# Kernel optimization log

Measured on AMD Instinct MI355X. Metric: run time of the kernel, lower is better.

## Reference

```python
import jax, jax.numpy as jnp
import numpy as np

N_EMBED = 1024
N_HEADS = 16
HEAD = N_EMBED // N_HEADS
EPS = 1e-5


def setup_inputs() -> dict:
    key = jax.random.key(0)
    ks = jax.random.split(key, 16)
    C = N_EMBED
    s = lambda fan_in: 1.0 / np.sqrt(fan_in)
    return {
        "x": jax.random.normal(ks[0], (4, 2048, C), jnp.float32),
        "ln1_g": jnp.ones((C,), jnp.float32),
        "ln1_b": jnp.zeros((C,), jnp.float32),
        "w_attn": jax.random.normal(ks[1], (C, 3 * C), jnp.float32) * s(C),
        "b_attn": jnp.zeros((3 * C,), jnp.float32),
        "w_proj": jax.random.normal(ks[2], (C, C), jnp.float32) * s(C),
        "b_proj": jnp.zeros((C,), jnp.float32),
        "ln2_g": jnp.ones((C,), jnp.float32),
        "ln2_b": jnp.zeros((C,), jnp.float32),
        "w_fc": jax.random.normal(ks[3], (C, 4 * C), jnp.float32) * s(C),
        "b_fc": jnp.zeros((4 * C,), jnp.float32),
        "w_fc2": jax.random.normal(ks[4], (4 * C, C), jnp.float32) * s(4 * C),
        "b_fc2": jnp.zeros((C,), jnp.float32),
    }


def _layernorm(x, g, b):
    mu = jnp.mean(x, axis=-1, keepdims=True)
    var = jnp.mean(jnp.square(x - mu), axis=-1, keepdims=True)
    return (x - mu) * jax.lax.rsqrt(var + EPS) * g + b


def _attention(x, w_attn, b_attn, w_proj, b_proj):
    B, T, C = x.shape
    qkv = x @ w_attn + b_attn  # [B,T,3C]
    q, k, v = jnp.split(qkv, 3, axis=-1)
    q = q.reshape(B, T, N_HEADS, HEAD).transpose(0, 2, 1, 3)  # [B,H,T,D]
    k = k.reshape(B, T, N_HEADS, HEAD).transpose(0, 2, 1, 3)
    v = v.reshape(B, T, N_HEADS, HEAD).transpose(0, 2, 1, 3)
    scale = 1.0 / np.sqrt(HEAD)
    affin = jnp.einsum("bhqd,bhkd->bhqk", q, k) * scale  # [B,H,T,T]
    causal = jnp.tril(jnp.ones((T, T), bool))
    affin = jnp.where(causal, affin, -jnp.inf)
    affin = jax.nn.softmax(affin, axis=-1)
    y = jnp.einsum("bhqk,bhkd->bhqd", affin, v)  # [B,H,T,D]
    y = y.transpose(0, 2, 1, 3).reshape(B, T, C)
    return y @ w_proj + b_proj


def reference(x, ln1_g, ln1_b, w_attn, b_attn, w_proj, b_proj,
              ln2_g, ln2_b, w_fc, b_fc, w_fc2, b_fc2):
    x = x + _attention(_layernorm(x, ln1_g, ln1_b), w_attn, b_attn, w_proj, b_proj)
    h = _layernorm(x, ln2_g, ln2_b)
    h = jax.nn.gelu(h @ w_fc + b_fc, approximate=True)  # tanh GELU
    x = x + (h @ w_fc2 + b_fc2)
    return x
```

## Files before the change

### kernel.cpp

```cpp
#include <hip/hip_runtime.h>
#include <math.h>


#define M_ROWS 8192
#define T_SEQ 2048
#define N_EMB 1024
#define N_HEADS 16
#define HEAD_D 64

typedef _Float16 f16;
typedef __attribute__((ext_vector_type(8))) _Float16 f16x8;
typedef __attribute__((ext_vector_type(4))) _Float16 f16x4;
typedef __attribute__((ext_vector_type(4))) float f32x4;

__device__ __forceinline__ void async16(void* lds, const void* g) {
    __builtin_amdgcn_global_load_lds(
        (const __attribute__((address_space(1))) unsigned int*)g,
        (__attribute__((address_space(3))) unsigned int*)lds, 16, 0, 0);
}

__device__ __forceinline__ float gelu_tanh(float v) {
    float u = 0.7978845608028654f * (v + 0.044715f * v * v * v);
    float e = __expf(2.0f * u);
    float t = 1.0f - 2.0f / (e + 1.0f);
    return 0.5f * v * (1.0f + t);
}

__launch_bounds__(256)
__global__ void wconv_kernel(const float* __restrict__ W, f16* __restrict__ WT,
                             int K, int N) {
    __shared__ float t[32][33];
    int tx = threadIdx.x & 31, ty = threadIdx.x >> 5;
    int n0 = blockIdx.x * 32, k0 = blockIdx.y * 32;
    #pragma unroll
    for (int r = 0; r < 4; r++)
        t[ty * 4 + r][tx] = W[(size_t)(k0 + ty * 4 + r) * N + n0 + tx];
    __syncthreads();
    #pragma unroll
    for (int r = 0; r < 4; r++)
        WT[(size_t)(n0 + ty * 4 + r) * K + k0 + tx] = (f16)t[tx][ty * 4 + r];
}

__launch_bounds__(256)
__global__ void ln_kernel(const float* __restrict__ x, const float* __restrict__ g,
                          const float* __restrict__ b, f16* __restrict__ y) {
    int row = blockIdx.x;
    int tid = threadIdx.x;
    const float* xr = x + (size_t)row * N_EMB;
    float4 v = *(const float4*)(xr + tid * 4);
    float s  = v.x + v.y + v.z + v.w;
    float sq = v.x * v.x + v.y * v.y + v.z * v.z + v.w * v.w;
    #pragma unroll
    for (int off = 32; off > 0; off >>= 1) {
        s  += __shfl_down(s, off);
        sq += __shfl_down(sq, off);
    }
    __shared__ float ws_[4], wq_[4];
    __shared__ float mean_s, rstd_s;
    int lane = tid & 63, wid = tid >> 6;
    if (lane == 0) { ws_[wid] = s; wq_[wid] = sq; }
    __syncthreads();
    if (tid == 0) {
        float st = ws_[0] + ws_[1] + ws_[2] + ws_[3];
        float qt = wq_[0] + wq_[1] + wq_[2] + wq_[3];
        float mu = st * (1.0f / N_EMB);
        float var = qt * (1.0f / N_EMB) - mu * mu;
        mean_s = mu;
        rstd_s = rsqrtf(var + 1e-5f);
    }
    __syncthreads();
    float mu = mean_s, r = rstd_s;
    float4 gv = *(const float4*)(g + tid * 4);
    float4 bv = *(const float4*)(b + tid * 4);
    f16x4 o;
    o.x = (f16)((v.x - mu) * r * gv.x + bv.x);
    o.y = (f16)((v.y - mu) * r * gv.y + bv.y);
    o.z = (f16)((v.z - mu) * r * gv.z + bv.z);
    o.w = (f16)((v.w - mu) * r * gv.w + bv.w);
    *(f16x4*)(y + (size_t)row * N_EMB + tid * 4) = o;
}

template <int EPI>
__launch_bounds__(256)
__global__ void gemm_f16(const f16* __restrict__ A, const f16* __restrict__ Bt,
                         const float* __restrict__ bias, const float* __restrict__ res,
                         float* __restrict__ Cf, f16* __restrict__ Ch,
                         f16* __restrict__ vT, int K, int N) {
    __shared__ f16 As[3][128 * 32];
    __shared__ f16 Bs[3][128 * 32];
    int tid = threadIdx.x;
    int lane = tid & 63, wave = tid >> 6;
    int wr = wave >> 1, wc = wave & 1;
    int quad = lane >> 4, l16 = lane & 15;

    int nx = gridDim.x;
    int nwg = nx * gridDim.y;
    int orig = blockIdx.y * nx + blockIdx.x;
    int cpx = nwg >> 3;
    int swz = (orig & 7) * cpx + (orig >> 3);
    int m0 = (swz / nx) * 128, n0 = (swz % nx) * 128;

    int r0 = tid >> 2;
    int s0 = (tid & 3) * 8;
    const f16* paA0 = A  + (size_t)(m0 + r0) * K + s0;
    const f16* paA1 = A  + (size_t)(m0 + r0 + 64) * K + s0;
    const f16* paB0 = Bt + (size_t)(n0 + r0) * K + s0;
    const f16* paB1 = Bt + (size_t)(n0 + r0 + 64) * K + s0;
    char* sA0 = (char*)As + (size_t)tid * 16;
    char* sA1 = (char*)As + (size_t)(256 + tid) * 16;
    char* sB0 = (char*)Bs + (size_t)tid * 16;
    char* sB1 = (char*)Bs + (size_t)(256 + tid) * 16;

    int nt = K >> 5;

    {
        async16(sA0, paA0); async16(sA1, paA1);
        async16(sB0, paB0); async16(sB1, paB1);
        async16(sA0 + 8192, paA0 + 32); async16(sA1 + 8192, paA1 + 32);
        async16(sB0 + 8192, paB0 + 32); async16(sB1 + 8192, paB1 + 32);
    }

    f32x4 acc[4][4] = {};
    int bc = 0;
    for (int t = 0; t < nt; t++) {
        if (t + 2 < nt) {
            int b2 = bc ? bc - 1 : 2;
            size_t bo = (size_t)b2 * 8192;
            int koff = (t + 2) * 32;
            async16(sA0 + bo, paA0 + koff); async16(sA1 + bo, paA1 + koff);
            async16(sB0 + bo, paB0 + koff); async16(sB1 + bo, paB1 + koff);
            asm volatile("s_waitcnt vmcnt(8)" ::: "memory");
        } else if (t + 2 == nt) {
            asm volatile("s_waitcnt vmcnt(4)" ::: "memory");
        } else {
            asm volatile("s_waitcnt vmcnt(0)" ::: "memory");
        }
        __builtin_amdgcn_s_barrier();

        const f16* as = As[bc];
        const f16* bs = Bs[bc];
        f16x8 af[4], bf[4];
        #pragma unroll
        for (int i = 0; i < 4; i++)
            af[i] = *(const f16x8*)&as[(wr * 64 + i * 16 + l16) * 32 + quad * 8];
        #pragma unroll
        for (int j = 0; j < 4; j++)
            bf[j] = *(const f16x8*)&bs[(wc * 64 + j * 16 + l16) * 32 + quad * 8];
        __builtin_amdgcn_s_setprio(1);
        #pragma unroll
        for (int i = 0; i < 4; i++)
            #pragma unroll
            for (int j = 0; j < 4; j++)
                acc[i][j] = __builtin_amdgcn_mfma_f32_16x16x32_f16(
                    af[i], bf[j], acc[i][j], 0, 0, 0);
        __builtin_amdgcn_s_setprio(0);
        __builtin_amdgcn_s_barrier();
        bc = (bc == 2) ? 0 : bc + 1;
    }

    #pragma unroll
    for (int i = 0; i < 4; i++) {
        int row0 = m0 + wr * 64 + i * 16 + quad * 4;
        #pragma unroll
        for (int j = 0; j < 4; j++) {
            int col = n0 + wc * 64 + j * 16 + l16;
            float bb = bias[col];
            if (EPI == 3) {
                if (n0 < 2048) {
                    #pragma unroll
                    for (int r = 0; r < 4; r++)
                        Ch[(size_t)(row0 + r) * 2048 + col] = (f16)(acc[i][j][r] + bb);
                } else {
                    int hh = (col - 2048) >> 6, dd = col & 63;
                    int bb_ = row0 >> 11, t0 = row0 & 2047;
                    f16x4 pk;
                    pk.x = (f16)(acc[i][j][0] + bb);
                    pk.y = (f16)(acc[i][j][1] + bb);
                    pk.z = (f16)(acc[i][j][2] + bb);
                    pk.w = (f16)(acc[i][j][3] + bb);
                    *(f16x4*)(vT + ((size_t)(bb_ * 16 + hh) * 64 + dd) * 2048 + t0) = pk;
                }
            } else {
                #pragma unroll
                for (int r = 0; r < 4; r++) {
                    size_t idx = (size_t)(row0 + r) * N + col;
                    float v = acc[i][j][r] + bb;
                    if (EPI == 1) v += res[idx];
                    if (EPI == 2) Ch[idx] = (f16)gelu_tanh(v);
                    else          Cf[idx] = v;
                }
            }
        }
    }
}

__launch_bounds__(256, 2)
__global__ void flash_kernel(const f16* __restrict__ qk, const f16* __restrict__ vT,
                             f16* __restrict__ y) {
    __shared__ __align__(16) char smem[67584];
    f16* Ks = (f16*)smem;
    f16* Vs = (f16*)(smem + 16384);
    int tid = threadIdx.x;
    int lane = tid & 63, w = tid >> 6;
    int quad = lane >> 4, l16 = lane & 15;
    f16* Ps = (f16*)(smem + 32768 + w * 8704);

    int bh = blockIdx.y;
    int b = bh >> 4, h = bh & 15;

    for (int half = 0; half < 2; half++) {
        int qt = half ? (int)blockIdx.x : 15 - (int)blockIdx.x;
        int q0 = qt * 128;

        f16x8 qf[2][2];
        #pragma unroll
        for (int qn = 0; qn < 2; qn++) {
            int q = q0 + w * 32 + qn * 16 + l16;
            #pragma unroll
            for (int dblk = 0; dblk < 2; dblk++) {
                f16x8 t = *(const f16x8*)(qk + (size_t)(b * T_SEQ + q) * 2048 +
                                          h * 64 + dblk * 32 + quad * 8);
                #pragma unroll
                for (int e = 0; e < 8; e++) t[e] = t[e] * (f16)0.125f;
                qf[qn][dblk] = t;
            }
        }

        float m_r[2] = {-INFINITY, -INFINITY};
        float l_r[2] = {0.0f, 0.0f};
        f32x4 Oacc[2][4] = {};

        for (int jt = 0; jt <= qt; jt++) {
            int j0 = jt * 128;
            __syncthreads();
            #pragma unroll
            for (int i = 0; i < 4; i++) {
                int L = i * 256 + tid;
                int j = L >> 3, g1 = L & 7;
                int g = g1 ^ (j & 7);
                async16((char*)Ks + (size_t)L * 16,
                        qk + (size_t)(b * T_SEQ + j0 + j) * 2048 + 1024 + h * 64 + g * 8);
            }
            #pragma unroll
            for (int i = 0; i < 4; i++) {
                int L = i * 256 + tid;
                int d = L >> 4, g1 = L & 15;
                int g = (g1 & 8) | ((g1 ^ d) & 7);
                async16((char*)Vs + (size_t)L * 16,
                        vT + ((size_t)(bh) * 64 + d) * 2048 + j0 + g * 8);
            }
            __syncthreads();

            f32x4 S[8][2];
            #pragma unroll
            for (int jm = 0; jm < 8; jm++) {
                f16x8 kf[2];
                #pragma unroll
                for (int dblk = 0; dblk < 2; dblk++) {
                    int j = jm * 16 + l16;
                    int g = (dblk * 4 + quad) ^ (j & 7);
                    kf[dblk] = *(const f16x8*)(Ks + (size_t)(j * 8 + g) * 8);
                }
                #pragma unroll
                for (int qn = 0; qn < 2; qn++) {
                    f32x4 s = {};
                    s = __builtin_amdgcn_mfma_f32_16x16x32_f16(kf[0], qf[qn][0], s, 0, 0, 0);
                    s = __builtin_amdgcn_mfma_f32_16x16x32_f16(kf[1], qf[qn][1], s, 0, 0, 0);
                    S[jm][qn] = s;
                }
            }

            if (jt == qt) {
                #pragma unroll
                for (int jm = 0; jm < 8; jm++)
                    #pragma unroll
                    for (int qn = 0; qn < 2; qn++)
                        #pragma unroll
                        for (int r = 0; r < 4; r++) {
                            int jl = jm * 16 + quad * 4 + r;
                            int ql = w * 32 + qn * 16 + l16;
                            if (jl > ql) S[jm][qn][r] = -1e30f;
                        }
            }

            float alpha[2];
            #pragma unroll
            for (int qn = 0; qn < 2; qn++) {
                float tmax = -INFINITY;
                #pragma unroll
                for (int jm = 0; jm < 8; jm++)
                    #pragma unroll
                    for (int r = 0; r < 4; r++)
                        tmax = fmaxf(tmax, S[jm][qn][r]);
                tmax = fmaxf(tmax, __shfl_xor(tmax, 16));
                tmax = fmaxf(tmax, __shfl_xor(tmax, 32));
                float mnew = fmaxf(m_r[qn], tmax);
                alpha[qn] = __expf(m_r[qn] - mnew);
                m_r[qn] = mnew;
                float rsum = 0.0f;
                #pragma unroll
                for (int jm = 0; jm < 8; jm++)
                    #pragma unroll
                    for (int r = 0; r < 4; r++) {
                        float p = __expf(S[jm][qn][r] - mnew);
                        S[jm][qn][r] = p;
                        rsum += p;
                    }
                rsum += __shfl_xor(rsum, 16);
                rsum += __shfl_xor(rsum, 32);
                l_r[qn] = l_r[qn] * alpha[qn] + rsum;
            }

            #pragma unroll
            for (int jm = 0; jm < 8; jm++)
                #pragma unroll
                for (int qn = 0; qn < 2; qn++) {
                    f16x4 pk;
                    pk.x = (f16)S[jm][qn][0];
                    pk.y = (f16)S[jm][qn][1];
                    pk.z = (f16)S[jm][qn][2];
                    pk.w = (f16)S[jm][qn][3];
                    *(f16x4*)(Ps + (size_t)(qn * 16 + l16) * 136 + jm * 16 + quad * 4) = pk;
                }

            float aPV[2][4];
            #pragma unroll
            for (int m = 0; m < 2; m++)
                #pragma unroll
                for (int r = 0; r < 4; r++)
                    aPV[m][r] = __shfl(alpha[m], quad * 20 + r);
            #pragma unroll
            for (int m = 0; m < 2; m++)
                #pragma unroll
                for (int n = 0; n < 4; n++)
                    #pragma unroll
                    for (int r = 0; r < 4; r++)
                        Oacc[m][n][r] *= aPV[m][r];

            #pragma unroll
            for (int kblk = 0; kblk < 4; kblk++) {
                f16x8 pf[2];
                #pragma unroll
                for (int m = 0; m < 2; m++)
                    pf[m] = *(const f16x8*)(Ps + (size_t)(m * 16 + l16) * 136 +
                                            kblk * 32 + quad * 8);
                f16x8 vf[4];
                #pragma unroll
                for (int n = 0; n < 4; n++) {
                    int d = n * 16 + l16;
                    int g = (kblk * 4 + quad);
                    int gs = (g & 8) | ((g ^ d) & 7);
                    vf[n] = *(const f16x8*)(Vs + (size_t)(d * 16 + gs) * 8);
                }
                #pragma unroll
                for (int m = 0; m < 2; m++)
                    #pragma unroll
                    for (int n = 0; n < 4; n++)
                        Oacc[m][n] = __builtin_amdgcn_mfma_f32_16x16x32_f16(
                            pf[m], vf[n], Oacc[m][n], 0, 0, 0);
            }
        }

        #pragma unroll
        for (int m = 0; m < 2; m++) {
            float lPV[4];
            #pragma unroll
            for (int r = 0; r < 4; r++)
                lPV[r] = 1.0f / __shfl(l_r[m], quad * 20 + r);
            #pragma unroll
            for (int n = 0; n < 4; n++) {
                #pragma unroll
                for (int r = 0; r < 4; r++) {
                    int q = q0 + w * 32 + m * 16 + quad * 4 + r;
                    y[(size_t)(b * T_SEQ + q) * N_EMB + h * 64 + n * 16 + l16] =
                        (f16)(Oacc[m][n][r] * lPV[r]);
                }
            }
        }
    }
}

extern "C" void kernel_launch(void* const* d_in, const int* in_sizes, int n_in,
                              void* d_out, int out_size, void* d_ws, size_t ws_size,
                              hipStream_t stream) {
    const float* x      = (const float*)d_in[0];
    const float* ln1_g  = (const float*)d_in[1];
    const float* ln1_b  = (const float*)d_in[2];
    const float* w_attn = (const float*)d_in[3];
    const float* b_attn = (const float*)d_in[4];
    const float* w_proj = (const float*)d_in[5];
    const float* b_proj = (const float*)d_in[6];
    const float* ln2_g  = (const float*)d_in[7];
    const float* ln2_b  = (const float*)d_in[8];
    const float* w_fc   = (const float*)d_in[9];
    const float* b_fc   = (const float*)d_in[10];
    const float* w_fc2  = (const float*)d_in[11];
    const float* b_fc2  = (const float*)d_in[12];
    float* out = (float*)d_out;

    const size_t MB = 1024 * 1024;
    char* ws = (char*)d_ws;
    f16*   lnbuf = (f16*)ws;
    f16*   qkbuf = (f16*)(ws + 16 * MB);
    f16*   vTbuf = (f16*)(ws + 48 * MB);
    f16*   ybuf  = (f16*)(ws + 64 * MB);
    f16*   h     = (f16*)(ws + 80 * MB);
    f16*   wT    = (f16*)(ws + 144 * MB);
    f16* wT_attn = wT;
    f16* wT_proj = wT_attn + (size_t)3072 * 1024;
    f16* wT_fc   = wT_proj + (size_t)1024 * 1024;
    f16* wT_fc2  = wT_fc   + (size_t)1024 * 4096;

    wconv_kernel<<<dim3(3072 / 32, 1024 / 32), 256, 0, stream>>>(w_attn, wT_attn, 1024, 3072);
    wconv_kernel<<<dim3(1024 / 32, 1024 / 32), 256, 0, stream>>>(w_proj, wT_proj, 1024, 1024);
    wconv_kernel<<<dim3(4096 / 32, 1024 / 32), 256, 0, stream>>>(w_fc,   wT_fc,   1024, 4096);
    wconv_kernel<<<dim3(1024 / 32, 4096 / 32), 256, 0, stream>>>(w_fc2,  wT_fc2,  4096, 1024);

    ln_kernel<<<M_ROWS, 256, 0, stream>>>(x, ln1_g, ln1_b, lnbuf);
    gemm_f16<3><<<dim3(3072 / 128, M_ROWS / 128), 256, 0, stream>>>(
        lnbuf, wT_attn, b_attn, nullptr, nullptr, qkbuf, vTbuf, 1024, 3072);
    flash_kernel<<<dim3(8, 64), 256, 0, stream>>>(qkbuf, vTbuf, ybuf);
    gemm_f16<1><<<dim3(1024 / 128, M_ROWS / 128), 256, 0, stream>>>(
        ybuf, wT_proj, b_proj, x, out, nullptr, nullptr, 1024, 1024);
    ln_kernel<<<M_ROWS, 256, 0, stream>>>(out, ln2_g, ln2_b, lnbuf);
    gemm_f16<2><<<dim3(4096 / 128, M_ROWS / 128), 256, 0, stream>>>(
        lnbuf, wT_fc, b_fc, nullptr, nullptr, h, nullptr, 1024, 4096);
    gemm_f16<1><<<dim3(1024 / 128, M_ROWS / 128), 256, 0, stream>>>(
        h, wT_fc2, b_fc2, out, out, nullptr, nullptr, 4096, 1024);
}
```

Before: 523.7 us.

## Enlarge GEMM tile to 256x128 with swizzled LDS and split prefetch

The GEMM tile grows from 128x128 to 256x128, so each wave computes 128x64 with twice the accumulators. This reuses each B fragment across more MFMAs and halves the grid. LDS reads now use an XOR swizzle to avoid bank conflicts. Global-to-LDS prefetches are split into two batches placed between the two MFMA halves, which lets the trailing barrier be dropped. The larger register footprint and the 2-block launch bound risk spills or lower occupancy, and halving the M grid for the N=1024 GEMMs leaves only 256 workgroups.

```diff
diff --git a/kernel.cpp b/kernel.cpp
--- a/kernel.cpp
+++ b/kernel.cpp
@@ -81,12 +81,12 @@
 }
 
 template <int EPI>
-__launch_bounds__(256)
+__launch_bounds__(256, 2)
 __global__ void gemm_f16(const f16* __restrict__ A, const f16* __restrict__ Bt,
                          const float* __restrict__ bias, const float* __restrict__ res,
                          float* __restrict__ Cf, f16* __restrict__ Ch,
                          f16* __restrict__ vT, int K, int N) {
-    __shared__ f16 As[3][128 * 32];
+    __shared__ f16 As[3][256 * 32];
     __shared__ f16 Bs[3][128 * 32];
     int tid = threadIdx.x;
     int lane = tid & 63, wave = tid >> 6;
@@ -98,54 +98,54 @@
     int orig = blockIdx.y * nx + blockIdx.x;
     int cpx = nwg >> 3;
     int swz = (orig & 7) * cpx + (orig >> 3);
-    int m0 = (swz / nx) * 128, n0 = (swz % nx) * 128;
-
-    int r0 = tid >> 2;
-    int s0 = (tid & 3) * 8;
-    const f16* paA0 = A  + (size_t)(m0 + r0) * K + s0;
-    const f16* paA1 = A  + (size_t)(m0 + r0 + 64) * K + s0;
-    const f16* paB0 = Bt + (size_t)(n0 + r0) * K + s0;
-    const f16* paB1 = Bt + (size_t)(n0 + r0 + 64) * K + s0;
-    char* sA0 = (char*)As + (size_t)tid * 16;
-    char* sA1 = (char*)As + (size_t)(256 + tid) * 16;
-    char* sB0 = (char*)Bs + (size_t)tid * 16;
-    char* sB1 = (char*)Bs + (size_t)(256 + tid) * 16;
+    int m0 = (swz / nx) * 256, n0 = (swz % nx) * 128;
+
+    int srow = tid >> 2;
+    int sg = (tid & 3) ^ (srow & 3);
+    const f16* pA = A  + (size_t)(m0 + srow) * K + sg * 8;
+    const f16* pB = Bt + (size_t)(n0 + srow) * K + sg * 8;
+    char* dA = (char*)As + (size_t)tid * 16;
+    char* dB = (char*)Bs + (size_t)tid * 16;
 
     int nt = K >> 5;
 
-    {
-        async16(sA0, paA0); async16(sA1, paA1);
-        async16(sB0, paB0); async16(sB1, paB1);
-        async16(sA0 + 8192, paA0 + 32); async16(sA1 + 8192, paA1 + 32);
-        async16(sB0 + 8192, paB0 + 32); async16(sB1 + 8192, paB1 + 32);
-    }
-
-    f32x4 acc[4][4] = {};
-    int bc = 0;
+    #pragma unroll
+    for (int r = 0; r < 4; r++) async16(dA + r * 4096, pA + (size_t)(r * 64) * K);
+    #pragma unroll
+    for (int r = 0; r < 2; r++) async16(dB + r * 4096, pB + (size_t)(r * 64) * K);
+    #pragma unroll
+    for (int r = 0; r < 4; r++) async16(dA + 16384 + r * 4096, pA + (size_t)(r * 64) * K + 32);
+    #pragma unroll
+    for (int r = 0; r < 2; r++) async16(dB + 8192  + r * 4096, pB + (size_t)(r * 64) * K + 32);
+
+    f32x4 acc[8][4] = {};
+    int cswz = (quad ^ (l16 & 3)) * 8;
+    int bufr = 0;
     for (int t = 0; t < nt; t++) {
-        if (t + 2 < nt) {
-            int b2 = bc ? bc - 1 : 2;
-            size_t bo = (size_t)b2 * 8192;
-            int koff = (t + 2) * 32;
-            async16(sA0 + bo, paA0 + koff); async16(sA1 + bo, paA1 + koff);
-            async16(sB0 + bo, paB0 + koff); async16(sB1 + bo, paB1 + koff);
-            asm volatile("s_waitcnt vmcnt(8)" ::: "memory");
-        } else if (t + 2 == nt) {
-            asm volatile("s_waitcnt vmcnt(4)" ::: "memory");
-        } else {
-            asm volatile("s_waitcnt vmcnt(0)" ::: "memory");
-        }
+        if (t + 1 < nt) asm volatile("s_waitcnt vmcnt(6)" ::: "memory");
+        else            asm volatile("s_waitcnt vmcnt(0)" ::: "memory");
         __builtin_amdgcn_s_barrier();
 
-        const f16* as = As[bc];
-        const f16* bs = Bs[bc];
-        f16x8 af[4], bf[4];
+        const f16* as = As[bufr];
+        const f16* bs = Bs[bufr];
+        int bn = bufr + 2 >= 3 ? bufr - 1 : bufr + 2;
+        bool pf = (t + 2 < nt);
+        size_t koff = (size_t)(t + 2) * 32;
+
+        f16x8 bf[4];
+        #pragma unroll
+        for (int j = 0; j < 4; j++)
+            bf[j] = *(const f16x8*)&bs[(wc * 64 + j * 16 + l16) * 32 + cswz];
+
+        if (pf) {
+            async16(dA + bn * 16384,        pA + koff);
+            async16(dA + bn * 16384 + 4096, pA + (size_t)64 * K + koff);
+            async16(dA + bn * 16384 + 8192, pA + (size_t)128 * K + koff);
+        }
+        f16x8 af[4];
         #pragma unroll
         for (int i = 0; i < 4; i++)
-            af[i] = *(const f16x8*)&as[(wr * 64 + i * 16 + l16) * 32 + quad * 8];
-        #pragma unroll
-        for (int j = 0; j < 4; j++)
-            bf[j] = *(const f16x8*)&bs[(wc * 64 + j * 16 + l16) * 32 + quad * 8];
+            af[i] = *(const f16x8*)&as[(wr * 128 + i * 16 + l16) * 32 + cswz];
         __builtin_amdgcn_s_setprio(1);
         #pragma unroll
         for (int i = 0; i < 4; i++)
@@ -154,13 +154,30 @@
                 acc[i][j] = __builtin_amdgcn_mfma_f32_16x16x32_f16(
                     af[i], bf[j], acc[i][j], 0, 0, 0);
         __builtin_amdgcn_s_setprio(0);
-        __builtin_amdgcn_s_barrier();
-        bc = (bc == 2) ? 0 : bc + 1;
+
+        if (pf) {
+            async16(dA + bn * 16384 + 12288, pA + (size_t)192 * K + koff);
+            async16(dB + bn * 8192,          pB + koff);
+            async16(dB + bn * 8192 + 4096,   pB + (size_t)64 * K + koff);
+        }
+        #pragma unroll
+        for (int i = 0; i < 4; i++)
+            af[i] = *(const f16x8*)&as[(wr * 128 + (4 + i) * 16 + l16) * 32 + cswz];
+        __builtin_amdgcn_s_setprio(1);
+        #pragma unroll
+        for (int i = 0; i < 4; i++)
+            #pragma unroll
+            for (int j = 0; j < 4; j++)
+                acc[4 + i][j] = __builtin_amdgcn_mfma_f32_16x16x32_f16(
+                    af[i], bf[j], acc[4 + i][j], 0, 0, 0);
+        __builtin_amdgcn_s_setprio(0);
+
+        bufr = bufr + 1 >= 3 ? 0 : bufr + 1;
     }
 
     #pragma unroll
-    for (int i = 0; i < 4; i++) {
-        int row0 = m0 + wr * 64 + i * 16 + quad * 4;
+    for (int i = 0; i < 8; i++) {
+        int row0 = m0 + wr * 128 + i * 16 + quad * 4;
         #pragma unroll
         for (int j = 0; j < 4; j++) {
             int col = n0 + wc * 64 + j * 16 + l16;
@@ -417,14 +434,14 @@
     wconv_kernel<<<dim3(1024 / 32, 4096 / 32), 256, 0, stream>>>(w_fc2,  wT_fc2,  4096, 1024);
 
     ln_kernel<<<M_ROWS, 256, 0, stream>>>(x, ln1_g, ln1_b, lnbuf);
-    gemm_f16<3><<<dim3(3072 / 128, M_ROWS / 128), 256, 0, stream>>>(
+    gemm_f16<3><<<dim3(3072 / 128, M_ROWS / 256), 256, 0, stream>>>(
         lnbuf, wT_attn, b_attn, nullptr, nullptr, qkbuf, vTbuf, 1024, 3072);
     flash_kernel<<<dim3(8, 64), 256, 0, stream>>>(qkbuf, vTbuf, ybuf);
-    gemm_f16<1><<<dim3(1024 / 128, M_ROWS / 128), 256, 0, stream>>>(
+    gemm_f16<1><<<dim3(1024 / 128, M_ROWS / 256), 256, 0, stream>>>(
         ybuf, wT_proj, b_proj, x, out, nullptr, nullptr, 1024, 1024);
     ln_kernel<<<M_ROWS, 256, 0, stream>>>(out, ln2_g, ln2_b, lnbuf);
-    gemm_f16<2><<<dim3(4096 / 128, M_ROWS / 128), 256, 0, stream>>>(
+    gemm_f16<2><<<dim3(4096 / 128, M_ROWS / 256), 256, 0, stream>>>(
         lnbuf, wT_fc, b_fc, nullptr, nullptr, h, nullptr, 1024, 4096);
-    gemm_f16<1><<<dim3(1024 / 128, M_ROWS / 128), 256, 0, stream>>>(
+    gemm_f16<1><<<dim3(1024 / 128, M_ROWS / 256), 256, 0, stream>>>(
         h, wT_fc2, b_fc2, out, out, nullptr, nullptr, 4096, 1024);
 }
```

Result: slower. 591.7 us (+13.0%).
